# Optimization experiments

Measured on AMD Instinct MI355X. Metric: run time of the kernel, lower is better.

Reference implementation:

```python
import jax, jax.numpy as jnp
import numpy as np

B, N, D = 8, 1024, 256
H = 8
DH = D // H
R = 4          # relation types 0..3; adj value 4 = no relation
FF = 1024
EPS = 1e-5


def _lin(k, fan_in, shape):
    return jax.random.normal(k, shape, jnp.float32) * (1.0 / np.sqrt(fan_in))


def setup_inputs() -> dict:
    key = jax.random.key(0)
    ks = jax.random.split(key, 16)
    src = jax.random.normal(ks[0], (B, N, D), jnp.float32)
    adj_matrix = jax.random.randint(ks[1], (B, N, N), 0, 5, dtype=jnp.int32)
    Wq = _lin(ks[2], D, (D, D)); bq = jnp.zeros((D,), jnp.float32)
    Wk = _lin(ks[3], D, (D, D)); bk = jnp.zeros((D,), jnp.float32)
    Wv = _lin(ks[4], D, (R, D, D)); bv = jnp.zeros((R, D), jnp.float32)
    Wo = _lin(ks[5], D, (D, D)); bo = jnp.zeros((D,), jnp.float32)
    W1 = _lin(ks[6], D, (D, FF)); b1 = jnp.zeros((FF,), jnp.float32)
    W2 = _lin(ks[7], FF, (FF, D)); b2 = jnp.zeros((D,), jnp.float32)
    g1 = jnp.ones((D,), jnp.float32); beta1 = jnp.zeros((D,), jnp.float32)
    g2 = jnp.ones((D,), jnp.float32); beta2 = jnp.zeros((D,), jnp.float32)
    return dict(src=src, adj_matrix=adj_matrix, Wq=Wq, bq=bq, Wk=Wk, bk=bk,
                Wv=Wv, bv=bv, Wo=Wo, bo=bo, W1=W1, b1=b1, W2=W2, b2=b2,
                g1=g1, beta1=beta1, g2=g2, beta2=beta2)


def _ln(x, g, b):
    m = x.mean(-1, keepdims=True)
    v = ((x - m) ** 2).mean(-1, keepdims=True)
    return (x - m) * jax.lax.rsqrt(v + EPS) * g + b


def reference(src, adj_matrix, Wq, bq, Wk, bk, Wv, bv, Wo, bo, W1, b1, W2, b2, g1, beta1, g2, beta2):
    Bb, Nn, Dm = src.shape
    h, dh = H, Dm // H
    q = (src @ Wq + bq).reshape(Bb, Nn, h, dh).transpose(0, 2, 1, 3)  # (B,H,N,dh)
    k = (src @ Wk + bk).reshape(Bb, Nn, h, dh).transpose(0, 2, 1, 3)
    scores = jnp.einsum('bhid,bhjd->bhij', q, k) / np.sqrt(dh)
    attn = jax.nn.softmax(scores, axis=-1)                             # (B,H,N,N)
    out = jnp.zeros_like(q)
    for r in range(Wv.shape[0]):  # small fixed relation loop, matches module
        v_r = (src @ Wv[r] + bv[r]).reshape(Bb, Nn, h, dh).transpose(0, 2, 1, 3)
        mask = (adj_matrix == r)[:, None]                              # (B,1,N,N)
        out = out + jnp.einsum('bhij,bhjd->bhid', attn * mask, v_r)
    attn_out = out.transpose(0, 2, 1, 3).reshape(Bb, Nn, Dm) @ Wo + bo
    x = _ln(src + attn_out, g1, beta1)
    ff = jax.nn.gelu(x @ W1 + b1, approximate=False) @ W2 + b2
    return _ln(x + ff, g2, beta2)
```

## Files before the change

kernel.cpp:

```cpp
#include <hip/hip_runtime.h>
#include <hip/hip_bf16.h>
#include <cmath>

constexpr int CB  = 8;
constexpr int CN  = 1024;
constexpr int CD  = 256;
constexpr int CH  = 8;
constexpr int CDH = 32;
constexpr int CR  = 4;
constexpr int CFF = 1024;
constexpr float CEPS = 1e-5f;
constexpr float CS = 0.25503480f;
constexpr size_t SZH = (size_t)CB * CH * CN * CDH;

#define MODE_QK    0
#define MODE_FFN1  2
#define MODE_VT    4

typedef float v4f __attribute__((ext_vector_type(4)));
typedef short v8s __attribute__((ext_vector_type(8)));

static __device__ __forceinline__ short f2bf(float f) {
    unsigned u = __builtin_bit_cast(unsigned, f);
    u += 0x7fff + ((u >> 16) & 1);
    return (short)(u >> 16);
}
static __device__ __forceinline__ float bf2f(short s) {
    unsigned u = ((unsigned)(unsigned short)s) << 16;
    return __builtin_bit_cast(float, u);
}
static __device__ __forceinline__ unsigned cvtpk_bf16(float lo, float hi) {
    unsigned r;
    asm("v_cvt_pk_bf16_f32 %0, %1, %2" : "=v"(r) : "v"(lo), "v"(hi));
    return r;
}

static __device__ __forceinline__ void async_copy16(const void* g, void* l) {
    __builtin_amdgcn_global_load_lds(
        (const __attribute__((address_space(1))) void*)g,
        (__attribute__((address_space(3))) void*)l, 16, 0, 0);
}


template<int BM, int BN, int MODE>
__device__ __forceinline__ void gemm_body(
    const short* __restrict__ A, const short* __restrict__ Bw,
    const float* __restrict__ biasv, void* __restrict__ dest,
    int M, int K, int Nw, int bx, int by, short* smem)
{
    constexpr int WTM = BM / 2, WTN = BN / 2;
    constexpr int TM = WTM / 16, TN = WTN / 16;
    short* As = smem;
    short* Bs = smem + 2 * BM * 32;

    const int t    = threadIdx.x;
    const int lane = t & 63;
    const int w    = t >> 6;
    const int quad = lane >> 4, l15 = lane & 15;
    const int wm = w >> 1, wn = w & 1;
    const int m0 = bx * BM, n0 = by * BN;

    const int srow = lane >> 2;
    const int scol = (lane & 3) * 8;

    v4f acc[TM][TN];
    #pragma unroll
    for (int i = 0; i < TM; ++i)
        #pragma unroll
        for (int j = 0; j < TN; ++j) acc[i][j] = (v4f){0.f, 0.f, 0.f, 0.f};

    const int NK = K >> 5;

    auto stage = [&](int buf, int kt) {
        #pragma unroll
        for (int u = 0; u < BM / 64; ++u) {
            const int e0 = (w * (BM / 64) + u) * 512;
            const int row = (e0 >> 5) + srow;
            async_copy16(A + (size_t)(m0 + row) * K + kt + scol,
                         &As[buf * BM * 32 + e0]);
        }
        #pragma unroll
        for (int u = 0; u < BN / 64; ++u) {
            const int e0 = (w * (BN / 64) + u) * 512;
            const int row = (e0 >> 5) + srow;
            async_copy16(Bw + (size_t)(n0 + row) * K + kt + scol,
                         &Bs[buf * BN * 32 + e0]);
        }
    };

    stage(0, 0);

    for (int it = 0; it < NK; ++it) {
        __syncthreads();
        if (it + 1 < NK) stage((it + 1) & 1, (it + 1) << 5);

        const int buf = it & 1;
        v8s af[TM], bfr[TN];
        #pragma unroll
        for (int i = 0; i < TM; ++i)
            af[i] = *(const v8s*)&As[buf * BM * 32 +
                                     (wm * WTM + i * 16 + l15) * 32 + quad * 8];
        #pragma unroll
        for (int j = 0; j < TN; ++j)
            bfr[j] = *(const v8s*)&Bs[buf * BN * 32 +
                                      (wn * WTN + j * 16 + l15) * 32 + quad * 8];
        #pragma unroll
        for (int i = 0; i < TM; ++i)
            #pragma unroll
            for (int j = 0; j < TN; ++j)
                acc[i][j] = __builtin_amdgcn_mfma_f32_16x16x32_bf16(
                    af[i], bfr[j], acc[i][j], 0, 0, 0);
    }

    #pragma unroll
    for (int i = 0; i < TM; ++i) {
        #pragma unroll
        for (int j = 0; j < TN; ++j) {
            const int mb = m0 + wm * WTM + i * 16 + quad * 4;
            const int n  = n0 + wn * WTN + j * 16 + l15;
            float vals[4];
            if (MODE == MODE_VT) {
                #pragma unroll
                for (int rr = 0; rr < 4; ++rr) vals[rr] = acc[i][j][rr] + biasv[mb + rr];
            } else {
                #pragma unroll
                for (int rr = 0; rr < 4; ++rr) vals[rr] = acc[i][j][rr] + biasv[n];
            }

            if (MODE == MODE_QK) {
                if (n0 < 256) {
                    #pragma unroll
                    for (int rr = 0; rr < 4; ++rr) vals[rr] *= CS;
                }
                const int b = mb >> 10, ii0 = mb & 1023;
                const int plane = n >> 8, nn = n & 255;
                const int h = nn >> 5, d = nn & 31;
                #pragma unroll
                for (int rr = 0; rr < 4; ++rr)
                    ((short*)dest)[(size_t)plane * SZH +
                        (((size_t)(b * CH + h)) * CN + ii0 + rr) * CDH + d] =
                        f2bf(vals[rr]);
            } else if (MODE == MODE_VT) {
                const int b = n >> 10, ii = n & 1023;
                const int jj = ii & 63;
                const int cc = (((jj >> 4) & 1) << 5) | (((jj >> 2) & 3) << 3) |
                               (((jj >> 5) & 1) << 2) | (jj & 3);
                const int iip = (ii & ~63) | cc;
                #pragma unroll
                for (int rr = 0; rr < 4; ++rr) {
                    const int m = mb + rr;
                    const int r2 = m >> 8, hd = m & 255;
                    const int h = hd >> 5, d = hd & 31;
                    ((short*)dest)[2 * SZH +
                        (((size_t)(r2 * 64 + b * CH + h)) * CDH + d) * CN + iip] =
                        f2bf(vals[rr]);
                }
            } else {
                #pragma unroll
                for (int rr = 0; rr < 4; ++rr) {
                    const size_t idx = (size_t)(mb + rr) * Nw + n;
                    const float xx = vals[rr];
                    const float E = exp2f(2.302217f * (xx + 0.044715f * xx * xx * xx));
                    ((short*)dest)[idx] = f2bf(xx * E / (E + 1.f));
                }
            }
        }
    }
}

template<int BM, int BN, int MODE>
__global__ __launch_bounds__(256)
void gemm_mfma(const short* __restrict__ A, const short* __restrict__ Bw,
               const float* __restrict__ biasv, void* __restrict__ dest,
               int M, int K, int Nw)
{
    extern __shared__ short smem[];
    gemm_body<BM, BN, MODE>(A, Bw, biasv, dest, M, K, Nw,
                            blockIdx.x, blockIdx.y, smem);
}

__global__ __launch_bounds__(256)
void proj_kernel(const short* __restrict__ src_bf, const short* __restrict__ wqkvT,
                 const float* __restrict__ bpack, short* __restrict__ qkv,
                 const int* __restrict__ adj, unsigned char* __restrict__ adjsel)
{
    extern __shared__ short smem[];
    const int g = blockIdx.x;
    if (g < 256) {
        gemm_body<128, 128, MODE_QK>(src_bf, wqkvT, bpack, qkv,
                                     8192, 256, 512, g >> 2, g & 3, smem);
    } else if (g < 768) {
        const int h2 = g - 256;
        gemm_body<128, 128, MODE_VT>(wqkvT + 512 * 256, src_bf, bpack + 512,
                                     qkv, 1024, 256, 8192, h2 & 7, h2 >> 3, smem);
    } else {
        const int nout = CB * CN * CN / 8;
        for (int i = (g - 768) * 256 + threadIdx.x; i < nout; i += 512 * 256) {
            const int dwi = i & 127;
            const int row = i >> 7;
            const int T   = dwi >> 3, kq = dwi & 7;
            const int j0  = T * 64 + (kq & 3) * 4 + (kq >> 2) * 16;
            const int* p = adj + (size_t)row * CN + j0;
            const int4 q0 = *(const int4*)(p);
            const int4 q1 = *(const int4*)(p + 32);
            int2 o;
            o.x = (q0.x & 0xff) | ((q0.y & 0xff) << 8) |
                  ((q0.z & 0xff) << 16) | ((q0.w & 0xff) << 24);
            o.y = (q1.x & 0xff) | ((q1.y & 0xff) << 8) |
                  ((q1.z & 0xff) << 16) | ((q1.w & 0xff) << 24);
            ((int2*)adjsel)[i] = o;
        }
    }
}

template<bool OUTF, bool OUTB, bool ADDBF>
__global__ __launch_bounds__(256)
void gemm_ln32(const short* __restrict__ A, const short* __restrict__ Bw,
               const float* __restrict__ biasv, const void* __restrict__ addp,
               const float* __restrict__ gw, const float* __restrict__ be,
               float* __restrict__ outf, short* __restrict__ outb, int K)
{
    __shared__ short As[2][16 * 64];
    __shared__ short Bs[2][256 * 64];
    __shared__ float redS[16][4], redQ[16][4];

    const int t    = threadIdx.x;
    const int lane = t & 63;
    const int w    = t >> 6;
    const int quad = lane >> 4, l15 = lane & 15;
    const int m0   = blockIdx.x * 16;
    const int xsw  = l15 & 7;

    v4f acc[4];
    #pragma unroll
    for (int j = 0; j < 4; ++j) acc[j] = (v4f){0.f, 0.f, 0.f, 0.f};

    const int NK = K >> 6;

    auto stage = [&](int buf, int kt) {
        if (t < 128) {
            const int row = t >> 3, gc = t & 7;
            async_copy16(A + (size_t)(m0 + row) * K + kt + ((gc ^ (row & 7)) * 8),
                         &As[buf][t * 8]);
        }
        #pragma unroll
        for (int u = 0; u < 8; ++u) {
            const int gl = t + 256 * u;
            const int row = gl >> 3, gc = gl & 7;
            async_copy16(Bw + (size_t)row * K + kt + ((gc ^ (row & 7)) * 8),
                         &Bs[buf][gl * 8]);
        }
    };

    stage(0, 0);

    for (int it = 0; it < NK; ++it) {
        __syncthreads();
        if (it + 1 < NK) stage((it + 1) & 1, (it + 1) << 6);

        const int buf = it & 1;
        #pragma unroll
        for (int half = 0; half < 2; ++half) {
            const int gr = (quad + 4 * half) ^ xsw;
            const v8s af = *(const v8s*)&As[buf][l15 * 64 + gr * 8];
            #pragma unroll
            for (int j = 0; j < 4; ++j) {
                const v8s bfr = *(const v8s*)&Bs[buf][(w * 64 + 16 * j + l15) * 64 + gr * 8];
                acc[j] = __builtin_amdgcn_mfma_f32_16x16x32_bf16(af, bfr, acc[j], 0, 0, 0);
            }
        }
    }

    float v[4][4];
    #pragma unroll
    for (int rr = 0; rr < 4; ++rr) {
        const int row = m0 + quad * 4 + rr;
        float s = 0.f, sq = 0.f;
        #pragma unroll
        for (int j = 0; j < 4; ++j) {
            const int n = w * 64 + 16 * j + l15;
            const size_t idx = (size_t)row * CD + n;
            const float addv = ADDBF ? bf2f(((const short*)addp)[idx])
                                     : ((const float*)addp)[idx];
            const float x = acc[j][rr] + biasv[n] + addv;
            v[rr][j] = x;
            s += x; sq += x * x;
        }
        #pragma unroll
        for (int off = 1; off < 16; off <<= 1) {
            s  += __shfl_xor(s, off);
            sq += __shfl_xor(sq, off);
        }
        if (l15 == 0) {
            redS[quad * 4 + rr][w] = s;
            redQ[quad * 4 + rr][w] = sq;
        }
    }
    __syncthreads();

    #pragma unroll
    for (int rr = 0; rr < 4; ++rr) {
        const int r16 = quad * 4 + rr;
        const int row = m0 + r16;
        const float s  = (redS[r16][0] + redS[r16][1]) + (redS[r16][2] + redS[r16][3]);
        const float sq = (redQ[r16][0] + redQ[r16][1]) + (redQ[r16][2] + redQ[r16][3]);
        const float mean = s * (1.f / CD);
        const float var  = sq * (1.f / CD) - mean * mean;
        const float rstd = rsqrtf(var + CEPS);
        #pragma unroll
        for (int j = 0; j < 4; ++j) {
            const int n = w * 64 + 16 * j + l15;
            const float y = (v[rr][j] - mean) * rstd * gw[n] + be[n];
            if (OUTF) outf[(size_t)row * CD + n] = y;
            if (OUTB) outb[(size_t)row * CD + n] = f2bf(y);
        }
    }
}

__global__ __launch_bounds__(256)
void prep(const float* __restrict__ src,
          const float* __restrict__ Wq, const float* __restrict__ Wk,
          const float* __restrict__ Wv, const float* __restrict__ Wo,
          const float* __restrict__ W1, const float* __restrict__ W2,
          const float* __restrict__ bq, const float* __restrict__ bk,
          const float* __restrict__ bv, const float* __restrict__ bo,
          const float* __restrict__ b1, const float* __restrict__ b2,
          short* __restrict__ src_bf,
          short* __restrict__ wqkvT, short* __restrict__ woT,
          short* __restrict__ w1T, short* __restrict__ w2T,
          float* __restrict__ bpack)
{
    __shared__ float tile[64][65];
    const int bx = blockIdx.x, t = threadIdx.x;
    if (bx < 2048) {
        const int i = bx * 256 + t;
        const float4 v = ((const float4*)src)[i];
        short4 o;
        o.x = f2bf(v.x); o.y = f2bf(v.y); o.z = f2bf(v.z); o.w = f2bf(v.w);
        ((short4*)src_bf)[i] = o;
    } else if (bx < 2288) {
        const int tt = bx - 2048;
        const float* S; short* D;
        int Sstride, Dstride, k0, srccol, dstrow;
        if (tt < 96) {
            const int tk = tt & 3, tn = tt >> 2;
            const int ng = tn * 64;
            Sstride = 256; Dstride = 256; k0 = tk * 64;
            dstrow = tn * 64; D = wqkvT;
            if (ng < 256)      { S = Wq; srccol = ng; }
            else if (ng < 512) { S = Wk; srccol = ng - 256; }
            else { const int r = (ng - 512) >> 8;
                   S = Wv + (size_t)r * 65536; srccol = (ng - 512) & 255; }
        } else if (tt < 112) {
            const int u = tt - 96, tk = u & 3, tn = u >> 2;
            S = Wo; Sstride = 256; D = woT; Dstride = 256;
            k0 = tk * 64; srccol = tn * 64; dstrow = tn * 64;
        } else if (tt < 176) {
            const int u = tt - 112, tk = u & 3, tn = u >> 2;
            S = W1; Sstride = 1024; D = w1T; Dstride = 256;
            k0 = tk * 64; srccol = tn * 64; dstrow = tn * 64;
        } else {
            const int u = tt - 176, tk = u & 15, tn = u >> 4;
            S = W2; Sstride = 256; D = w2T; Dstride = 1024;
            k0 = tk * 64; srccol = tn * 64; dstrow = tn * 64;
        }
        #pragma unroll
        for (int u2 = 0; u2 < 4; ++u2) {
            const int kl = (t >> 4) + u2 * 16;
            const int nl = (t & 15) * 4;
            const float4 v = *(const float4*)&S[(size_t)(k0 + kl) * Sstride + srccol + nl];
            tile[kl][nl + 0] = v.x; tile[kl][nl + 1] = v.y;
            tile[kl][nl + 2] = v.z; tile[kl][nl + 3] = v.w;
        }
        __syncthreads();
        #pragma unroll
        for (int u2 = 0; u2 < 4; ++u2) {
            const int nl = (t >> 4) + u2 * 16;
            const int kl = (t & 15) * 4;
            short4 o;
            o.x = f2bf(tile[kl + 0][nl]); o.y = f2bf(tile[kl + 1][nl]);
            o.z = f2bf(tile[kl + 2][nl]); o.w = f2bf(tile[kl + 3][nl]);
            *(short4*)&D[(size_t)(dstrow + nl) * Dstride + k0 + kl] = o;
        }
    } else {
        const int idx = (bx - 2288) * 256 + t;
        float bvv;
        if (idx < 256)       bvv = bq[idx];
        else if (idx < 512)  bvv = bk[idx - 256];
        else if (idx < 1536) bvv = bv[idx - 512];
        else if (idx < 1792) bvv = bo[idx - 1536];
        else if (idx < 2816) bvv = b1[idx - 1792];
        else                 bvv = b2[idx - 2816];
        bpack[idx] = bvv;
    }
}

__global__ __launch_bounds__(256, 4)
void attn_mfma(const short* __restrict__ qg, const short* __restrict__ kg,
               const short* __restrict__ vt, const unsigned char* __restrict__ adjsel,
               short* __restrict__ outh)
{
    __shared__ __align__(16) short vtl[2][8192];

    const int t    = threadIdx.x;
    const int lane = t & 63;
    const int w    = t >> 6;
    const int quad = lane >> 4;
    const int l15  = lane & 15;
    const int g    = blockIdx.x;
    const int b    = g & 7;
    const int h    = (g >> 3) & 7;
    const int i0   = (g >> 6) * 64;
    const int bhh  = b * CH + h;
    const size_t bh = (size_t)bhh;

    const v8s qfrag = *(const v8s*)&qg[(bh * CN + i0 + 16 * w + l15) * CDH + quad * 8];

    const short* vsrc[4];
    #pragma unroll
    for (int u = 0; u < 4; ++u) {
        const int gl = t + 256 * u;
        const int r = gl >> 8, d = (gl >> 3) & 31, gc = gl & 7;
        vsrc[u] = vt + ((size_t)(r * 64 + bhh) * CDH + d) * CN + (gc ^ (d & 7)) * 8;
    }
    const short* kbase = kg + (bh * CN + l15) * CDH + quad * 8;
    const unsigned char* abase =
        adjsel + ((size_t)(b * CN) + i0 + 16 * w + l15) * CN + quad * 8;

    v4f oacc[2][2];
    #pragma unroll
    for (int cb = 0; cb < 2; ++cb)
        #pragma unroll
        for (int kb = 0; kb < 2; ++kb) oacc[cb][kb] = (v4f){0.f, 0.f, 0.f, 0.f};
    float plsum = 0.f;
    const int psw = (l15 & 7) * 8;

    #pragma unroll
    for (int u = 0; u < 4; ++u)
        async_copy16(vsrc[u], &vtl[0][(t + 256 * u) * 8]);
    v8s kpre[4];
    #pragma unroll
    for (int jb = 0; jb < 4; ++jb)
        kpre[jb] = *(const v8s*)(kbase + (16 * jb) * CDH);
    int2 apre0 = *(const int2*)(abase);
    int2 apre1 = *(const int2*)(abase + 32);

    for (int jt = 0; jt < 16; ++jt) {
        __syncthreads();
        const int p = jt & 1;

        v4f sacc[4];
        #pragma unroll
        for (int jb = 0; jb < 4; ++jb)
            sacc[jb] = __builtin_amdgcn_mfma_f32_16x16x32_bf16(
                kpre[jb], qfrag, (v4f){0.f, 0.f, 0.f, 0.f}, 0, 0, 0);

        const int2 a0 = apre0, a1 = apre1;
        const int jn = (jt + 1) & 15;
        #pragma unroll
        for (int u = 0; u < 4; ++u)
            async_copy16(vsrc[u] + jn * 64, &vtl[p ^ 1][(t + 256 * u) * 8]);
        #pragma unroll
        for (int jb = 0; jb < 4; ++jb)
            kpre[jb] = *(const v8s*)(kbase + (jn * 64 + 16 * jb) * CDH);
        apre0 = *(const int2*)(abase + jn * 64);
        apre1 = *(const int2*)(abase + jn * 64 + 32);

        float pv[4][4];
        #pragma unroll
        for (int jb = 0; jb < 4; ++jb)
            #pragma unroll
            for (int rr = 0; rr < 4; ++rr) pv[jb][rr] = exp2f(sacc[jb][rr]);
        plsum += ((pv[0][0] + pv[0][1]) + (pv[0][2] + pv[0][3]))
               + ((pv[1][0] + pv[1][1]) + (pv[1][2] + pv[1][3]))
               + ((pv[2][0] + pv[2][1]) + (pv[2][2] + pv[2][3]))
               + ((pv[3][0] + pv[3][1]) + (pv[3][2] + pv[3][3]));

        #pragma unroll
        for (int kb = 0; kb < 2; ++kb) {
            v8s vf[4][2];
            #pragma unroll
            for (int r = 0; r < 4; ++r)
                #pragma unroll
                for (int cb = 0; cb < 2; ++cb)
                    vf[r][cb] = *(const v8s*)&vtl[p][r * 2048 +
                        (16 * cb + l15) * 64 + (((4 * kb + quad) * 8) ^ psw)];

            const unsigned P[4] = {
                cvtpk_bf16(pv[kb][0],     pv[kb][1]),
                cvtpk_bf16(pv[kb][2],     pv[kb][3]),
                cvtpk_bf16(pv[kb + 2][0], pv[kb + 2][1]),
                cvtpk_bf16(pv[kb + 2][2], pv[kb + 2][3])};
            const int2 aa = kb ? a1 : a0;
            const unsigned D[4] = {
                __builtin_amdgcn_perm((unsigned)aa.x, (unsigned)aa.x, 0x01010000u),
                __builtin_amdgcn_perm((unsigned)aa.x, (unsigned)aa.x, 0x03030202u),
                __builtin_amdgcn_perm((unsigned)aa.y, (unsigned)aa.y, 0x01010000u),
                __builtin_amdgcn_perm((unsigned)aa.y, (unsigned)aa.y, 0x03030202u)};
            unsigned pfm[4][4];
            #pragma unroll
            for (int r = 0; r < 4; ++r) {
                const unsigned tb = 0xffu << (8 * r);
                #pragma unroll
                for (int u = 0; u < 4; ++u)
                    pfm[r][u] = P[u] & __builtin_amdgcn_perm(0u, tb, D[u]);
            }
            __builtin_amdgcn_s_setprio(1);
            #pragma unroll
            for (int r = 0; r < 4; ++r) {
                const v8s pfr = __builtin_bit_cast(v8s,
                    make_uint4(pfm[r][0], pfm[r][1], pfm[r][2], pfm[r][3]));
                #pragma unroll
                for (int cb = 0; cb < 2; ++cb)
                    oacc[cb][kb] = __builtin_amdgcn_mfma_f32_16x16x32_bf16(
                        pfr, vf[r][cb], oacc[cb][kb], 0, 0, 0);
            }
            __builtin_amdgcn_s_setprio(0);
        }
    }

    v4f ofin[2];
    ofin[0] = oacc[0][0] + oacc[0][1];
    ofin[1] = oacc[1][0] + oacc[1][1];
    float plF = plsum;
    plF += __shfl_xor(plF, 16);
    plF += __shfl_xor(plF, 32);
    #pragma unroll
    for (int rr = 0; rr < 4; ++rr) {
        const float inv = 1.f / __shfl(plF, quad * 4 + rr);
        const int row = i0 + 16 * w + quad * 4 + rr;
        #pragma unroll
        for (int cb = 0; cb < 2; ++cb)
            outh[((size_t)b * CN + row) * CD + h * CDH + 16 * cb + l15] =
                f2bf(ofin[cb][rr] * inv);
    }
}

extern "C" void kernel_launch(void* const* d_in, const int* in_sizes, int n_in,
                              void* d_out, int out_size, void* d_ws, size_t ws_size,
                              hipStream_t stream)
{
    const float* src = (const float*)d_in[0];
    const int*   adj = (const int*)d_in[1];
    const float* Wq  = (const float*)d_in[2];
    const float* bq  = (const float*)d_in[3];
    const float* Wk  = (const float*)d_in[4];
    const float* bk  = (const float*)d_in[5];
    const float* Wv  = (const float*)d_in[6];
    const float* bv  = (const float*)d_in[7];
    const float* Wo  = (const float*)d_in[8];
    const float* bo  = (const float*)d_in[9];
    const float* W1  = (const float*)d_in[10];
    const float* b1  = (const float*)d_in[11];
    const float* W2  = (const float*)d_in[12];
    const float* b2  = (const float*)d_in[13];
    const float* g1  = (const float*)d_in[14];
    const float* be1 = (const float*)d_in[15];
    const float* g2  = (const float*)d_in[16];
    const float* be2 = (const float*)d_in[17];
    float* out = (float*)d_out;

    char* wsb = (char*)d_ws;
    const size_t MB = (size_t)1 << 20;

    unsigned char* adjsel = (unsigned char*)(wsb);
    short* qkv_bf = (short*)(wsb + 8 * MB);
    short* src_bf = (short*)(wsb + 32 * MB);
    short* wqkvT  = (short*)(wsb + 36 * MB);
    short* woT    = (short*)(wsb + 36 * MB + 768 * 1024);
    short* w1T    = (short*)(wsb + 36 * MB + 896 * 1024);
    short* w2T    = (short*)(wsb + 36 * MB + 1408 * 1024);
    float* bpack  = (float*)(wsb + 36 * MB + 1920 * 1024);
    short* heads_bf = (short*)(wsb + 38 * MB);
    short* x_bf   = (short*)(wsb + 32 * MB);
    short* h1_bf  = (short*)(wsb + 16 * MB);

    const int M = CB * CN;
    dim3 blk(256);

    prep<<<dim3(2300), blk, 0, stream>>>(src, Wq, Wk, Wv, Wo, W1, W2,
        bq, bk, bv, bo, b1, b2, src_bf, wqkvT, woT, w1T, w2T, bpack);

    proj_kernel<<<dim3(1280), blk, 32768, stream>>>(
        src_bf, wqkvT, bpack, qkv_bf, adj, adjsel);

    attn_mfma<<<dim3(1024), blk, 0, stream>>>(
        qkv_bf, qkv_bf + SZH, qkv_bf + 2 * SZH, adjsel, heads_bf);

    gemm_ln32<false, true, false><<<dim3(M / 16), blk, 0, stream>>>(
        heads_bf, woT, bpack + 1536, src, g1, be1, nullptr, x_bf, CD);

    gemm_mfma<128, 128, MODE_FFN1><<<dim3(M / 128, CFF / 128), blk, 32768, stream>>>(
        x_bf, w1T, bpack + 1792, h1_bf, M, CD, CFF);

    gemm_ln32<true, false, true><<<dim3(M / 16), blk, 0, stream>>>(
        h1_bf, w2T, bpack + 2816, x_bf, g2, be2, out, nullptr, CFF);
}
```

Baseline: 216.8 us.

## Process two 64-row query tiles per attention block to reuse K/V loads

Each attention block now handles 128 query rows (two 64-row halves) instead of 64, so every K fragment and shared-memory V tile is loaded once and used for both halves. The grid is halved to 512 blocks and launch bounds drop to 2 blocks per SM to allow the extra accumulator and score registers. This cuts global and LDS traffic per query row, at the cost of lower occupancy and fewer blocks to spread across the CUs.

```diff
diff --git a/kernel.cpp b/kernel.cpp
--- a/kernel.cpp
+++ b/kernel.cpp
@@ -395,7 +395,7 @@
     }
 }
 
-__global__ __launch_bounds__(256, 4)
+__global__ __launch_bounds__(256, 2)
 void attn_mfma(const short* __restrict__ qg, const short* __restrict__ kg,
                const short* __restrict__ vt, const unsigned char* __restrict__ adjsel,
                short* __restrict__ outh)
@@ -410,11 +410,14 @@
     const int g    = blockIdx.x;
     const int b    = g & 7;
     const int h    = (g >> 3) & 7;
-    const int i0   = (g >> 6) * 64;
+    const int i0   = (g >> 6) * 128;
     const int bhh  = b * CH + h;
     const size_t bh = (size_t)bhh;
 
-    const v8s qfrag = *(const v8s*)&qg[(bh * CN + i0 + 16 * w + l15) * CDH + quad * 8];
+    v8s qfrag[2];
+    #pragma unroll
+    for (int hh = 0; hh < 2; ++hh)
+        qfrag[hh] = *(const v8s*)&qg[(bh * CN + i0 + 64 * hh + 16 * w + l15) * CDH + quad * 8];
 
     const short* vsrc[4];
     #pragma unroll
@@ -424,15 +427,19 @@
         vsrc[u] = vt + ((size_t)(r * 64 + bhh) * CDH + d) * CN + (gc ^ (d & 7)) * 8;
     }
     const short* kbase = kg + (bh * CN + l15) * CDH + quad * 8;
-    const unsigned char* abase =
-        adjsel + ((size_t)(b * CN) + i0 + 16 * w + l15) * CN + quad * 8;
-
-    v4f oacc[2][2];
-    #pragma unroll
-    for (int cb = 0; cb < 2; ++cb)
-        #pragma unroll
-        for (int kb = 0; kb < 2; ++kb) oacc[cb][kb] = (v4f){0.f, 0.f, 0.f, 0.f};
-    float plsum = 0.f;
+    const unsigned char* abase[2];
+    #pragma unroll
+    for (int hh = 0; hh < 2; ++hh)
+        abase[hh] = adjsel + ((size_t)(b * CN) + i0 + 64 * hh + 16 * w + l15) * CN + quad * 8;
+
+    v4f oacc[2][2][2];
+    #pragma unroll
+    for (int hh = 0; hh < 2; ++hh)
+        #pragma unroll
+        for (int cb = 0; cb < 2; ++cb)
+            #pragma unroll
+            for (int kb = 0; kb < 2; ++kb) oacc[hh][cb][kb] = (v4f){0.f, 0.f, 0.f, 0.f};
+    float plsum[2] = {0.f, 0.f};
     const int psw = (l15 & 7) * 8;
 
     #pragma unroll
@@ -442,20 +449,31 @@
     #pragma unroll
     for (int jb = 0; jb < 4; ++jb)
         kpre[jb] = *(const v8s*)(kbase + (16 * jb) * CDH);
-    int2 apre0 = *(const int2*)(abase);
-    int2 apre1 = *(const int2*)(abase + 32);
+    int2 apre[2][2];
+    #pragma unroll
+    for (int hh = 0; hh < 2; ++hh) {
+        apre[hh][0] = *(const int2*)(abase[hh]);
+        apre[hh][1] = *(const int2*)(abase[hh] + 32);
+    }
 
     for (int jt = 0; jt < 16; ++jt) {
         __syncthreads();
         const int p = jt & 1;
 
-        v4f sacc[4];
-        #pragma unroll
-        for (int jb = 0; jb < 4; ++jb)
-            sacc[jb] = __builtin_amdgcn_mfma_f32_16x16x32_bf16(
-                kpre[jb], qfrag, (v4f){0.f, 0.f, 0.f, 0.f}, 0, 0, 0);
-
-        const int2 a0 = apre0, a1 = apre1;
+        v4f sacc[2][4];
+        #pragma unroll
+        for (int hh = 0; hh < 2; ++hh)
+            #pragma unroll
+            for (int jb = 0; jb < 4; ++jb)
+                sacc[hh][jb] = __builtin_amdgcn_mfma_f32_16x16x32_bf16(
+                    kpre[jb], qfrag[hh], (v4f){0.f, 0.f, 0.f, 0.f}, 0, 0, 0);
+
+        int2 aa[2][2];
+        #pragma unroll
+        for (int hh = 0; hh < 2; ++hh) {
+            aa[hh][0] = apre[hh][0];
+            aa[hh][1] = apre[hh][1];
+        }
         const int jn = (jt + 1) & 15;
         #pragma unroll
         for (int u = 0; u < 4; ++u)
@@ -463,18 +481,24 @@
         #pragma unroll
         for (int jb = 0; jb < 4; ++jb)
             kpre[jb] = *(const v8s*)(kbase + (jn * 64 + 16 * jb) * CDH);
-        apre0 = *(const int2*)(abase + jn * 64);
-        apre1 = *(const int2*)(abase + jn * 64 + 32);
-
-        float pv[4][4];
-        #pragma unroll
-        for (int jb = 0; jb < 4; ++jb)
-            #pragma unroll
-            for (int rr = 0; rr < 4; ++rr) pv[jb][rr] = exp2f(sacc[jb][rr]);
-        plsum += ((pv[0][0] + pv[0][1]) + (pv[0][2] + pv[0][3]))
-               + ((pv[1][0] + pv[1][1]) + (pv[1][2] + pv[1][3]))
-               + ((pv[2][0] + pv[2][1]) + (pv[2][2] + pv[2][3]))
-               + ((pv[3][0] + pv[3][1]) + (pv[3][2] + pv[3][3]));
+        #pragma unroll
+        for (int hh = 0; hh < 2; ++hh) {
+            apre[hh][0] = *(const int2*)(abase[hh] + jn * 64);
+            apre[hh][1] = *(const int2*)(abase[hh] + jn * 64 + 32);
+        }
+
+        float pv[2][4][4];
+        #pragma unroll
+        for (int hh = 0; hh < 2; ++hh) {
+            #pragma unroll
+            for (int jb = 0; jb < 4; ++jb)
+                #pragma unroll
+                for (int rr = 0; rr < 4; ++rr) pv[hh][jb][rr] = exp2f(sacc[hh][jb][rr]);
+            plsum[hh] += ((pv[hh][0][0] + pv[hh][0][1]) + (pv[hh][0][2] + pv[hh][0][3]))
+                       + ((pv[hh][1][0] + pv[hh][1][1]) + (pv[hh][1][2] + pv[hh][1][3]))
+                       + ((pv[hh][2][0] + pv[hh][2][1]) + (pv[hh][2][2] + pv[hh][2][3]))
+                       + ((pv[hh][3][0] + pv[hh][3][1]) + (pv[hh][3][2] + pv[hh][3][3]));
+        }
 
         #pragma unroll
         for (int kb = 0; kb < 2; ++kb) {
@@ -486,53 +510,59 @@
                     vf[r][cb] = *(const v8s*)&vtl[p][r * 2048 +
                         (16 * cb + l15) * 64 + (((4 * kb + quad) * 8) ^ psw)];
 
-            const unsigned P[4] = {
-                cvtpk_bf16(pv[kb][0],     pv[kb][1]),
-                cvtpk_bf16(pv[kb][2],     pv[kb][3]),
-                cvtpk_bf16(pv[kb + 2][0], pv[kb + 2][1]),
-                cvtpk_bf16(pv[kb + 2][2], pv[kb + 2][3])};
-            const int2 aa = kb ? a1 : a0;
-            const unsigned D[4] = {
-                __builtin_amdgcn_perm((unsigned)aa.x, (unsigned)aa.x, 0x01010000u),
-                __builtin_amdgcn_perm((unsigned)aa.x, (unsigned)aa.x, 0x03030202u),
-                __builtin_amdgcn_perm((unsigned)aa.y, (unsigned)aa.y, 0x01010000u),
-                __builtin_amdgcn_perm((unsigned)aa.y, (unsigned)aa.y, 0x03030202u)};
-            unsigned pfm[4][4];
-            #pragma unroll
-            for (int r = 0; r < 4; ++r) {
-                const unsigned tb = 0xffu << (8 * r);
-                #pragma unroll
-                for (int u = 0; u < 4; ++u)
-                    pfm[r][u] = P[u] & __builtin_amdgcn_perm(0u, tb, D[u]);
+            #pragma unroll
+            for (int hh = 0; hh < 2; ++hh) {
+                const unsigned P[4] = {
+                    cvtpk_bf16(pv[hh][kb][0],     pv[hh][kb][1]),
+                    cvtpk_bf16(pv[hh][kb][2],     pv[hh][kb][3]),
+                    cvtpk_bf16(pv[hh][kb + 2][0], pv[hh][kb + 2][1]),
+                    cvtpk_bf16(pv[hh][kb + 2][2], pv[hh][kb + 2][3])};
+                const int2 a2 = aa[hh][kb];
+                const unsigned D[4] = {
+                    __builtin_amdgcn_perm((unsigned)a2.x, (unsigned)a2.x, 0x01010000u),
+                    __builtin_amdgcn_perm((unsigned)a2.x, (unsigned)a2.x, 0x03030202u),
+                    __builtin_amdgcn_perm((unsigned)a2.y, (unsigned)a2.y, 0x01010000u),
+                    __builtin_amdgcn_perm((unsigned)a2.y, (unsigned)a2.y, 0x03030202u)};
+                unsigned pfm[4][4];
+                #pragma unroll
+                for (int r = 0; r < 4; ++r) {
+                    const unsigned tb = 0xffu << (8 * r);
+                    #pragma unroll
+                    for (int u = 0; u < 4; ++u)
+                        pfm[r][u] = P[u] & __builtin_amdgcn_perm(0u, tb, D[u]);
+                }
+                __builtin_amdgcn_s_setprio(1);
+                #pragma unroll
+                for (int r = 0; r < 4; ++r) {
+                    const v8s pfr = __builtin_bit_cast(v8s,
+                        make_uint4(pfm[r][0], pfm[r][1], pfm[r][2], pfm[r][3]));
+                    #pragma unroll
+                    for (int cb = 0; cb < 2; ++cb)
+                        oacc[hh][cb][kb] = __builtin_amdgcn_mfma_f32_16x16x32_bf16(
+                            pfr, vf[r][cb], oacc[hh][cb][kb], 0, 0, 0);
+                }
+                __builtin_amdgcn_s_setprio(0);
             }
-            __builtin_amdgcn_s_setprio(1);
-            #pragma unroll
-            for (int r = 0; r < 4; ++r) {
-                const v8s pfr = __builtin_bit_cast(v8s,
-                    make_uint4(pfm[r][0], pfm[r][1], pfm[r][2], pfm[r][3]));
-                #pragma unroll
-                for (int cb = 0; cb < 2; ++cb)
-                    oacc[cb][kb] = __builtin_amdgcn_mfma_f32_16x16x32_bf16(
-                        pfr, vf[r][cb], oacc[cb][kb], 0, 0, 0);
-            }
-            __builtin_amdgcn_s_setprio(0);
-        }
-    }
-
-    v4f ofin[2];
-    ofin[0] = oacc[0][0] + oacc[0][1];
-    ofin[1] = oacc[1][0] + oacc[1][1];
-    float plF = plsum;
-    plF += __shfl_xor(plF, 16);
-    plF += __shfl_xor(plF, 32);
-    #pragma unroll
-    for (int rr = 0; rr < 4; ++rr) {
-        const float inv = 1.f / __shfl(plF, quad * 4 + rr);
-        const int row = i0 + 16 * w + quad * 4 + rr;
-        #pragma unroll
-        for (int cb = 0; cb < 2; ++cb)
-            outh[((size_t)b * CN + row) * CD + h * CDH + 16 * cb + l15] =
-                f2bf(ofin[cb][rr] * inv);
+        }
+    }
+
+    #pragma unroll
+    for (int hh = 0; hh < 2; ++hh) {
+        v4f ofin[2];
+        ofin[0] = oacc[hh][0][0] + oacc[hh][0][1];
+        ofin[1] = oacc[hh][1][0] + oacc[hh][1][1];
+        float plF = plsum[hh];
+        plF += __shfl_xor(plF, 16);
+        plF += __shfl_xor(plF, 32);
+        #pragma unroll
+        for (int rr = 0; rr < 4; ++rr) {
+            const float inv = 1.f / __shfl(plF, quad * 4 + rr);
+            const int row = i0 + 64 * hh + 16 * w + quad * 4 + rr;
+            #pragma unroll
+            for (int cb = 0; cb < 2; ++cb)
+                outh[((size_t)b * CN + row) * CD + h * CDH + 16 * cb + l15] =
+                    f2bf(ofin[cb][rr] * inv);
+        }
     }
 }
 
@@ -584,7 +614,7 @@
     proj_kernel<<<dim3(1280), blk, 32768, stream>>>(
         src_bf, wqkvT, bpack, qkv_bf, adj, adjsel);
 
-    attn_mfma<<<dim3(1024), blk, 0, stream>>>(
+    attn_mfma<<<dim3(512), blk, 0, stream>>>(
         qkv_bf, qkv_bf + SZH, qkv_bf + 2 * SZH, adjsel, heads_bf);
 
     gemm_ln32<false, true, false><<<dim3(M / 16), blk, 0, stream>>>(
```

Measured after the change: 209.6 us. 3.3% less time.
